# Optimization experiments

Hardware: AMD Instinct MI355X
Metric: run time of the kernel (lower is better)

Reference implementation:

```python
import jax, jax.numpy as jnp
import numpy as np

N, E, H, L = 50000, 800000, 96, 4

def _gelu(x):
    return jax.nn.gelu(x, approximate=False)

def _mlp2(x, w1, b1, w2, b2):
    # Linear -> GELU -> (Dropout=identity in eval) -> Linear
    return _gelu(x @ w1 + b1) @ w2 + b2

def setup_inputs() -> dict:
    key = jax.random.key(0)
    ks = jax.random.split(key, 40)
    p = lambda k, s: jax.random.normal(k, s, jnp.float32) * 0.05
    inp = {
        'x': jax.random.normal(ks[0], (N, 6), jnp.float32),
        'edge_index': jax.random.randint(ks[1], (2, E), 0, N, jnp.int64),
        'edge_attr': jax.random.normal(ks[2], (E, 8), jnp.float32),
        # node encoder
        'ne_w1': p(ks[3], (6, H)), 'ne_b1': p(ks[4], (H,)),
        'ne_w2': p(ks[5], (H, H)), 'ne_b2': p(ks[6], (H,)),
        # edge encoder
        'ee_w1': p(ks[7], (8, H)), 'ee_b1': p(ks[8], (H,)),
        'ee_w2': p(ks[9], (H, H)), 'ee_b2': p(ks[10], (H,)),
        # per-layer message-passing MLPs (stacked over L)
        'mp_ew1': p(ks[11], (L, 3 * H, H)), 'mp_eb1': p(ks[12], (L, H)),
        'mp_ew2': p(ks[13], (L, H, H)),     'mp_eb2': p(ks[14], (L, H)),
        'mp_nw1': p(ks[15], (L, 2 * H, H)), 'mp_nb1': p(ks[16], (L, H)),
        'mp_nw2': p(ks[17], (L, H, H)),     'mp_nb2': p(ks[18], (L, H)),
        # node saliency head
        'nh_w1': p(ks[19], (H, H)), 'nh_b1': p(ks[20], (H,)),
        'nh_w2': p(ks[21], (H, 1)), 'nh_b2': p(ks[22], (1,)),
        # edge clustering head
        'eh_w1': p(ks[23], (3 * H, H)), 'eh_b1': p(ks[24], (H,)),
        'eh_w2': p(ks[25], (H, 1)),     'eh_b2': p(ks[26], (1,)),
    }
    return inp

def _forward(x, edge_attr, ne_w1, ne_b1, ne_w2, ne_b2, ee_w1, ee_b1, ee_w2, ee_b2,
             mp_ew1, mp_eb1, mp_ew2, mp_eb2, mp_nw1, mp_nb1, mp_nw2, mp_nb2,
             nh_w1, nh_b1, nh_w2, nh_b2, eh_w1, eh_b1, eh_w2, eh_b2, edge_index):
    src, dst = edge_index[0], edge_index[1]
    h = _mlp2(x, ne_w1, ne_b1, ne_w2, ne_b2)                 # [N,H]
    e = _mlp2(edge_attr, ee_w1, ee_b1, ee_w2, ee_b2)         # [E,H]
    for l in range(L):
        # edge update: residual MLP over [h_src, h_dst, e]
        m = jnp.concatenate([h[src], h[dst], e], axis=-1)    # [E,3H]
        e = e + _mlp2(m, mp_ew1[l], mp_eb1[l], mp_ew2[l], mp_eb2[l])
        # node update: residual MLP over [h, sum of incoming edge states]
        agg = jax.ops.segment_sum(e, dst, num_segments=N)    # [N,H]
        h = h + _mlp2(jnp.concatenate([h, agg], axis=-1), mp_nw1[l], mp_nb1[l], mp_nw2[l], mp_nb2[l])
    edge_logits = _mlp2(jnp.concatenate([h[src], h[dst], e], axis=-1), eh_w1, eh_b1, eh_w2, eh_b2)[:, 0]
    node_logits = _mlp2(h, nh_w1, nh_b1, nh_w2, nh_b2)[:, 0]
    return edge_logits, node_logits

def reference(x, edge_index, edge_attr, ne_w1, ne_b1, ne_w2, ne_b2, ee_w1, ee_b1, ee_w2, ee_b2,
              mp_ew1, mp_eb1, mp_ew2, mp_eb2, mp_nw1, mp_nb1, mp_nw2, mp_nb2,
              nh_w1, nh_b1, nh_w2, nh_b2, eh_w1, eh_b1, eh_w2, eh_b2):
    return _forward(x, edge_attr, ne_w1, ne_b1, ne_w2, ne_b2, ee_w1, ee_b1, ee_w2, ee_b2,
                    mp_ew1, mp_eb1, mp_ew2, mp_eb2, mp_nw1, mp_nb1, mp_nw2, mp_nb2,
                    nh_w1, nh_b1, nh_w2, nh_b2, eh_w1, eh_b1, eh_w2, eh_b2, edge_index)
```

## Files before the change

### kernel.cpp

```cpp
#include <hip/hip_runtime.h>
#include <hip/hip_bf16.h>
#include <math.h>


typedef __attribute__((ext_vector_type(8))) short short8;
typedef __attribute__((ext_vector_type(4))) float f32x4;

#define MFMA(a, b, c) __builtin_amdgcn_mfma_f32_16x16x32_bf16((a), (b), (c), 0, 0, 0)
#define WSTR 112

__device__ __forceinline__ float bf2f(ushort u) {
    union { uint i; float f; } v; v.i = ((uint)u) << 16; return v.f;
}
__device__ __forceinline__ ushort f2bf(float f) {
    union { float f; uint i; } v; v.f = f;
    uint b = v.i;
    return (ushort)((b + 0x7FFFu + ((b >> 16) & 1u)) >> 16);
}
__device__ __forceinline__ float gelu_f(float x) {
    return 0.5f * x * (1.0f + erff(x * 0.70710678118654752440f));
}
__device__ __forceinline__ short8 ld8(const ushort* p) { return *(const short8*)p; }
__device__ __forceinline__ ushort cvt_elem(const void* p, size_t j, int f32) {
    return f32 ? f2bf(((const float*)p)[j]) : ((const ushort*)p)[j];
}
template <int NT>
__device__ __forceinline__ void stageW(ushort* dst, const ushort* src, int t) {
    for (int i = t; i < 1152; i += NT) {
        int row = i / 12, ch = i - row * 12;
        ((short8*)dst)[row * 14 + ch] = ((const short8*)src)[i];
    }
}

__global__ __launch_bounds__(256) void detect_kernel(
    const ushort* __restrict__ X, const uint* __restrict__ IDX, int* __restrict__ flags)
{
    __shared__ int cnt[2];
    if (threadIdx.x == 0) { cnt[0] = 0; cnt[1] = 0; }
    __syncthreads();
    int plaus = 0;
    for (int i = threadIdx.x; i < 2048; i += 256) {
        float v = fabsf(bf2f(X[i]));
        if (v > 1e-3f && v < 100.f) plaus++;
    }
    atomicAdd(&cnt[0], plaus);
    int nz = 0;
    for (int i = threadIdx.x; i < 1024; i += 256)
        if (IDX[2 * i + 1] != 0) nz++;
    atomicAdd(&cnt[1], nz);
    __syncthreads();
    if (threadIdx.x == 0) {
        flags[0] = (cnt[0] < 1843) ? 1 : 0;
        flags[1] = (cnt[1] == 0) ? 1 : 0;
    }
}

struct SPk { const void* src[16]; int off[17]; };
__global__ __launch_bounds__(256) void smalls_kernel(SPk p, ushort* __restrict__ dst,
                                                     const int* __restrict__ flags) {
    int f = flags[0];
    for (int i = threadIdx.x; i < 3650; i += 256) {
        int e = 0;
        while (e < 15 && i >= p.off[e + 1]) e++;
        dst[i] = cvt_elem(p.src[e], (size_t)(i - p.off[e]), f);
    }
}

struct TPk { const void* base[34]; int eloff[34]; };
__global__ __launch_bounds__(256) void transpose_k(TPk p, ushort* __restrict__ dst,
                                                   const int* __restrict__ flags) {
    int f = flags[0];
    int m = blockIdx.x;
    const void* s = p.base[m];
    size_t off = (size_t)p.eloff[m];
    ushort* d = dst + (size_t)m * 9216;
    for (int i = threadIdx.x; i < 9216; i += 256) {
        int n = i / 96, k = i - n * 96;
        d[i] = cvt_elem(s, off + (size_t)k * 96 + n, f);
    }
}

__global__ __launch_bounds__(256) void idx_convert(
    const int* __restrict__ eidx, int* __restrict__ s32, int* __restrict__ d32,
    const int* __restrict__ flags, int E)
{
    int f = flags[1];
    for (size_t i = (size_t)blockIdx.x * 256 + threadIdx.x; i < (size_t)E;
         i += (size_t)gridDim.x * 256) {
        s32[i] = f ? eidx[2 * i] : eidx[i];
        d32[i] = f ? eidx[2 * ((size_t)E + i)] : eidx[(size_t)E + i];
    }
}

__global__ __launch_bounds__(256) void xe_convert(
    const void* __restrict__ xin, const void* __restrict__ ein,
    ushort* __restrict__ xb, ushort* __restrict__ eb,
    const int* __restrict__ flags, size_t nx, size_t ne)
{
    int f = flags[0];
    size_t total = nx + ne;
    for (size_t i = (size_t)blockIdx.x * 256 + threadIdx.x; i < total;
         i += (size_t)gridDim.x * 256) {
        if (i < nx) xb[i] = cvt_elem(xin, i, f);
        else        eb[i - nx] = cvt_elem(ein, i - nx, f);
    }
}

__global__ __launch_bounds__(256) void hist_kernel(const int* __restrict__ d32,
                                                   int* __restrict__ cnt, int E) {
    for (size_t i = (size_t)blockIdx.x * 256 + threadIdx.x; i < (size_t)E;
         i += (size_t)gridDim.x * 256)
        atomicAdd(&cnt[d32[i]], 1);
}

__global__ __launch_bounds__(1024) void prefix_kernel(int* __restrict__ cnt,
                                                      int* __restrict__ rowptr,
                                                      int N, int E) {
    __shared__ int part[1024];
    int t = threadIdx.x;
    int chunk = (N + 1023) / 1024;
    int b = t * chunk, e = b + chunk; if (e > N) e = N;
    int s = 0;
    for (int i = b; i < e; i++) s += cnt[i];
    part[t] = s;
    __syncthreads();
    for (int off = 1; off < 1024; off <<= 1) {
        int v = (t >= off) ? part[t - off] : 0;
        __syncthreads();
        part[t] += v;
        __syncthreads();
    }
    int run = part[t] - s;
    for (int i = b; i < e; i++) {
        int c = cnt[i];
        rowptr[i] = run;
        cnt[i] = run;
        run += c;
    }
    if (t == 1023) rowptr[N] = E;
}

__global__ __launch_bounds__(256) void scatter_kernel(
    const int* __restrict__ s32, const int* __restrict__ d32,
    int* __restrict__ cursor, int* __restrict__ ss, int* __restrict__ ds,
    int* __restrict__ eid, int E)
{
    for (size_t i = (size_t)blockIdx.x * 256 + threadIdx.x; i < (size_t)E;
         i += (size_t)gridDim.x * 256) {
        int d = d32[i];
        int pos = atomicAdd(&cursor[d], 1);
        ss[pos] = s32[i];
        ds[pos] = d;
        eid[pos] = (int)i;
    }
}

template <int K, bool WF32>
__global__ __launch_bounds__(256) void encoder_kernel(
    const ushort* __restrict__ X, const ushort* __restrict__ W1,
    const ushort* __restrict__ B1, const ushort* __restrict__ W2t,
    const ushort* __restrict__ B2, ushort* __restrict__ OutB,
    float* __restrict__ OutF, const int* __restrict__ EID, int R)
{
    __shared__ __align__(16) ushort sW2[96 * WSTR];
    __shared__ float sW1[K * 96];
    __shared__ float sb1[96], sb2[96];
    __shared__ __align__(16) ushort gscr[4][16 * WSTR];
    int t = threadIdx.x;
    stageW<256>(sW2, W2t, t);
    for (int i = t; i < K * 96; i += 256) sW1[i] = bf2f(W1[i]);
    if (t < 96) { sb1[t] = bf2f(B1[t]); sb2[t] = bf2f(B2[t]); }
    __syncthreads();

    const int wave = t >> 6, lane = t & 63, lr = lane & 15, cg = lane >> 4, lk = cg * 8;
    int rbase = blockIdx.x * 64 + wave * 16;

    float wf[K][6];
#pragma unroll
    for (int k = 0; k < K; k++)
#pragma unroll
        for (int n = 0; n < 6; n++) wf[k][n] = sW1[k * 96 + n * 16 + lr];

    ushort* g = gscr[wave];
#pragma unroll
    for (int j = 0; j < 4; j++) {
        int r = rbase + cg * 4 + j;
        int rc = r < R ? r : R - 1;
        int rx = EID ? EID[rc] : rc;
        float xr[K];
        const uint* xu = (const uint*)(X + (size_t)rx * K);
#pragma unroll
        for (int q = 0; q < K / 2; q++) {
            uint u = xu[q];
            xr[2 * q] = bf2f((ushort)u); xr[2 * q + 1] = bf2f((ushort)(u >> 16));
        }
#pragma unroll
        for (int n = 0; n < 6; n++) {
            float v = sb1[n * 16 + lr];
#pragma unroll
            for (int k = 0; k < K; k++) v += xr[k] * wf[k][n];
            g[(cg * 4 + j) * WSTR + n * 16 + lr] = f2bf(gelu_f(v));
        }
    }
    __syncthreads();

    const ushort* grow = g + lr * WSTR + lk;
    short8 a0 = ld8(grow), a1 = ld8(grow + 32), a2 = ld8(grow + 64);
    f32x4 acc[6];
#pragma unroll
    for (int n = 0; n < 6; n++) {
        f32x4 z = {0.f, 0.f, 0.f, 0.f}; acc[n] = z;
        const ushort* wb = sW2 + (n * 16 + lr) * WSTR + lk;
        acc[n] = MFMA(a0, ld8(wb), acc[n]);
        acc[n] = MFMA(a1, ld8(wb + 32), acc[n]);
        acc[n] = MFMA(a2, ld8(wb + 64), acc[n]);
    }
#pragma unroll
    for (int j = 0; j < 4; j++) {
        int r = rbase + cg * 4 + j;
        if (r < R) {
#pragma unroll
            for (int n = 0; n < 6; n++) {
                int c = n * 16 + lr;
                float v = acc[n][j] + sb2[c];
                OutB[(size_t)r * 96 + c] = f2bf(v);
                if constexpr (WF32) OutF[(size_t)r * 96 + c] = v;
            }
        }
    }
}

__global__ __launch_bounds__(256) void gemm_dual_kernel(
    const ushort* __restrict__ A, const ushort* __restrict__ W1t,
    const ushort* __restrict__ W2t, ushort* __restrict__ O1,
    ushort* __restrict__ O2, int R)
{
    __shared__ __align__(16) ushort sW1[96 * WSTR], sW2[96 * WSTR];
    int t = threadIdx.x;
    stageW<256>(sW1, W1t, t);
    stageW<256>(sW2, W2t, t);
    __syncthreads();
    const int wave = t >> 6, lane = t & 63, lr = lane & 15, cg = lane >> 4, lk = cg * 8;
    int rbase = blockIdx.x * 64 + wave * 16;
    int ra = rbase + lr; if (ra > R - 1) ra = R - 1;
    const ushort* arow = A + (size_t)ra * 96 + lk;
    short8 a0 = ld8(arow), a1 = ld8(arow + 32), a2 = ld8(arow + 64);
    f32x4 acc1[6], acc2[6];
#pragma unroll
    for (int n = 0; n < 6; n++) {
        f32x4 z = {0.f, 0.f, 0.f, 0.f}; acc1[n] = z; acc2[n] = z;
        const ushort* w1 = sW1 + (n * 16 + lr) * WSTR + lk;
        const ushort* w2 = sW2 + (n * 16 + lr) * WSTR + lk;
        acc1[n] = MFMA(a0, ld8(w1), acc1[n]);
        acc1[n] = MFMA(a1, ld8(w1 + 32), acc1[n]);
        acc1[n] = MFMA(a2, ld8(w1 + 64), acc1[n]);
        acc2[n] = MFMA(a0, ld8(w2), acc2[n]);
        acc2[n] = MFMA(a1, ld8(w2 + 32), acc2[n]);
        acc2[n] = MFMA(a2, ld8(w2 + 64), acc2[n]);
    }
#pragma unroll
    for (int j = 0; j < 4; j++) {
        int r = rbase + cg * 4 + j;
        if (r < R) {
#pragma unroll
            for (int n = 0; n < 6; n++) {
                int c = n * 16 + lr;
                O1[(size_t)r * 96 + c] = f2bf(acc1[n][j]);
                O2[(size_t)r * 96 + c] = f2bf(acc2[n][j]);
            }
        }
    }
}

__global__ __launch_bounds__(512) void edge_layer_kernel(
    ushort* __restrict__ Eio,
    const ushort* __restrict__ HA, const ushort* __restrict__ HB,
    const int* __restrict__ SRC, const int* __restrict__ DST,
    const ushort* __restrict__ W1t, const ushort* __restrict__ B1,
    const ushort* __restrict__ W2t, const ushort* __restrict__ B2,
    int ntiles, int Etot)
{
    __shared__ __align__(16) ushort sW1[96 * WSTR], sW2[96 * WSTR];
    __shared__ __align__(16) ushort gscr[8][16 * WSTR];
    __shared__ float sb1[96], sb2[96];
    int t = threadIdx.x;
    stageW<512>(sW1, W1t, t);
    stageW<512>(sW2, W2t, t);
    if (t < 96) { sb1[t] = bf2f(B1[t]); sb2[t] = bf2f(B2[t]); }
    __syncthreads();
    const int wave = t >> 6, lane = t & 63, lr = lane & 15, cg = lane >> 4, lk = cg * 8;
    ushort* g = gscr[wave];

    for (int tile = blockIdx.x; tile < ntiles; tile += gridDim.x) {
        int rbase = tile * 128 + wave * 16;
        int ra = rbase + lr; if (ra > Etot - 1) ra = Etot - 1;
        const ushort* arow = Eio + (size_t)ra * 96 + lk;
        short8 a0 = ld8(arow), a1 = ld8(arow + 32), a2 = ld8(arow + 64);
        f32x4 acc[6];
#pragma unroll
        for (int n = 0; n < 6; n++) {
            f32x4 z = {0.f, 0.f, 0.f, 0.f}; acc[n] = z;
            const ushort* wb = sW1 + (n * 16 + lr) * WSTR + lk;
            acc[n] = MFMA(a0, ld8(wb), acc[n]);
            acc[n] = MFMA(a1, ld8(wb + 32), acc[n]);
            acc[n] = MFMA(a2, ld8(wb + 64), acc[n]);
        }
        int s4[4], d4[4];
#pragma unroll
        for (int j = 0; j < 4; j++) {
            int r = rbase + cg * 4 + j; if (r > Etot - 1) r = Etot - 1;
            s4[j] = SRC[r]; d4[j] = DST[r];
        }
#pragma unroll
        for (int j = 0; j < 4; j++) {
            const ushort* pa = HA + (size_t)s4[j] * 96;
            const ushort* pb = HB + (size_t)d4[j] * 96;
            int rl = cg * 4 + j;
#pragma unroll
            for (int n = 0; n < 6; n++) {
                int c = n * 16 + lr;
                float v = acc[n][j] + bf2f(pa[c]) + bf2f(pb[c]) + sb1[c];
                g[rl * WSTR + c] = f2bf(gelu_f(v));
            }
        }
        __syncthreads();
        const ushort* grow = g + lr * WSTR + lk;
        short8 b0 = ld8(grow), b1v = ld8(grow + 32), b2v = ld8(grow + 64);
        f32x4 acc2[6];
#pragma unroll
        for (int n = 0; n < 6; n++) {
            f32x4 z = {0.f, 0.f, 0.f, 0.f}; acc2[n] = z;
            const ushort* wb = sW2 + (n * 16 + lr) * WSTR + lk;
            acc2[n] = MFMA(b0, ld8(wb), acc2[n]);
            acc2[n] = MFMA(b1v, ld8(wb + 32), acc2[n]);
            acc2[n] = MFMA(b2v, ld8(wb + 64), acc2[n]);
        }
#pragma unroll
        for (int j = 0; j < 4; j++) {
            int r = rbase + cg * 4 + j;
            if (r < Etot) {
                ushort* erow = Eio + (size_t)r * 96;
#pragma unroll
                for (int n = 0; n < 6; n++) {
                    int c = n * 16 + lr;
                    float v = acc2[n][j] + sb2[c] + bf2f(erow[c]);
                    erow[c] = f2bf(v);
                }
            }
        }
        __syncthreads();
    }
}

template <bool HF32>
__global__ __launch_bounds__(256) void node_layer_kernel(
    float* __restrict__ HF, ushort* __restrict__ HBF,
    const ushort* __restrict__ EB, const int* __restrict__ ROWPTR,
    const ushort* __restrict__ W1at, const ushort* __restrict__ W1bt,
    const ushort* __restrict__ B1, const ushort* __restrict__ W2t,
    const ushort* __restrict__ B2, int R)
{
    __shared__ __align__(16) ushort sWa[96 * WSTR], sWb[96 * WSTR], sW2[96 * WSTR];
    __shared__ __align__(16) ushort gscr[4][16 * WSTR];
    __shared__ float sb1[96], sb2[96];
    int t = threadIdx.x;
    stageW<256>(sWa, W1at, t);
    stageW<256>(sWb, W1bt, t);
    stageW<256>(sW2, W2t, t);
    if (t < 96) { sb1[t] = bf2f(B1[t]); sb2[t] = bf2f(B2[t]); }
    __syncthreads();
    const int wave = t >> 6, lane = t & 63, lr = lane & 15, cg = lane >> 4, lk = cg * 8;
    int rbase = blockIdx.x * 64 + wave * 16;
    int ra = rbase + lr; if (ra > R - 1) ra = R - 1;
    const ushort* hrow = HBF + (size_t)ra * 96 + lk;
    short8 a0 = ld8(hrow), a1 = ld8(hrow + 32), a2 = ld8(hrow + 64);

    float ag[24];
#pragma unroll
    for (int i = 0; i < 24; i++) ag[i] = 0.f;
    int beg = ROWPTR[ra], end = ROWPTR[ra + 1];
    for (int k = beg; k < end; k++) {
        const ushort* er = EB + (size_t)k * 96 + lk;
        short8 e0 = ld8(er), e1 = ld8(er + 32), e2 = ld8(er + 64);
#pragma unroll
        for (int i = 0; i < 8; i++) {
            ag[i]      += bf2f((ushort)e0[i]);
            ag[8 + i]  += bf2f((ushort)e1[i]);
            ag[16 + i] += bf2f((ushort)e2[i]);
        }
    }
    short8 g0, g1, g2;
#pragma unroll
    for (int i = 0; i < 8; i++) {
        g0[i] = (short)f2bf(ag[i]);
        g1[i] = (short)f2bf(ag[8 + i]);
        g2[i] = (short)f2bf(ag[16 + i]);
    }

    f32x4 acc[6];
#pragma unroll
    for (int n = 0; n < 6; n++) {
        f32x4 z = {0.f, 0.f, 0.f, 0.f}; acc[n] = z;
        const ushort* wa = sWa + (n * 16 + lr) * WSTR + lk;
        const ushort* wb = sWb + (n * 16 + lr) * WSTR + lk;
        acc[n] = MFMA(a0, ld8(wa), acc[n]);
        acc[n] = MFMA(a1, ld8(wa + 32), acc[n]);
        acc[n] = MFMA(a2, ld8(wa + 64), acc[n]);
        acc[n] = MFMA(g0, ld8(wb), acc[n]);
        acc[n] = MFMA(g1, ld8(wb + 32), acc[n]);
        acc[n] = MFMA(g2, ld8(wb + 64), acc[n]);
    }
    ushort* g = gscr[wave];
#pragma unroll
    for (int j = 0; j < 4; j++) {
        int rl = cg * 4 + j;
#pragma unroll
        for (int n = 0; n < 6; n++) {
            int c = n * 16 + lr;
            g[rl * WSTR + c] = f2bf(gelu_f(acc[n][j] + sb1[c]));
        }
    }
    __syncthreads();
    const ushort* grow = g + lr * WSTR + lk;
    short8 b0 = ld8(grow), b1v = ld8(grow + 32), b2v = ld8(grow + 64);
    f32x4 acc2[6];
#pragma unroll
    for (int n = 0; n < 6; n++) {
        f32x4 z = {0.f, 0.f, 0.f, 0.f}; acc2[n] = z;
        const ushort* wb = sW2 + (n * 16 + lr) * WSTR + lk;
        acc2[n] = MFMA(b0, ld8(wb), acc2[n]);
        acc2[n] = MFMA(b1v, ld8(wb + 32), acc2[n]);
        acc2[n] = MFMA(b2v, ld8(wb + 64), acc2[n]);
    }
#pragma unroll
    for (int j = 0; j < 4; j++) {
        int r = rbase + cg * 4 + j;
        if (r < R) {
#pragma unroll
            for (int n = 0; n < 6; n++) {
                int c = n * 16 + lr;
                size_t idx = (size_t)r * 96 + c;
                float base;
                if constexpr (HF32) base = HF[idx]; else base = bf2f(HBF[idx]);
                float v = base + acc2[n][j] + sb2[c];
                if constexpr (HF32) HF[idx] = v;
                HBF[idx] = f2bf(v);
            }
        }
    }
}

template <bool GATHER>
__global__ __launch_bounds__(256) void head_kernel(
    const ushort* __restrict__ Arows,
    const ushort* __restrict__ HA, const ushort* __restrict__ HB,
    const int* __restrict__ SRC, const int* __restrict__ DST,
    const ushort* __restrict__ W1t, const ushort* __restrict__ B1,
    const ushort* __restrict__ W2v, const ushort* __restrict__ B2,
    float* __restrict__ Out, const int* __restrict__ EID, int R)
{
    __shared__ __align__(16) ushort sW1[96 * WSTR];
    __shared__ float sb1[96], sw2[96];
    __shared__ float sb2s;
    int t = threadIdx.x;
    stageW<256>(sW1, W1t, t);
    if (t < 96) { sb1[t] = bf2f(B1[t]); sw2[t] = bf2f(W2v[t]); }
    if (t == 0) sb2s = bf2f(B2[0]);
    __syncthreads();
    const int wave = t >> 6, lane = t & 63, lr = lane & 15, cg = lane >> 4, lk = cg * 8;
    int rbase = blockIdx.x * 64 + wave * 16;
    int ra = rbase + lr; if (ra > R - 1) ra = R - 1;
    const ushort* arow = Arows + (size_t)ra * 96 + lk;
    short8 a0 = ld8(arow), a1 = ld8(arow + 32), a2 = ld8(arow + 64);

    f32x4 accT[6];
#pragma unroll
    for (int n = 0; n < 6; n++) {
        f32x4 z = {0.f, 0.f, 0.f, 0.f}; accT[n] = z;
        const ushort* wb = sW1 + (n * 16 + lr) * WSTR + lk;
        accT[n] = MFMA(ld8(wb), a0, accT[n]);
        accT[n] = MFMA(ld8(wb + 32), a1, accT[n]);
        accT[n] = MFMA(ld8(wb + 64), a2, accT[n]);
    }

    const ushort* pa = nullptr; const ushort* pb = nullptr;
    if constexpr (GATHER) {
        pa = HA + (size_t)SRC[ra] * 96 + cg * 4;
        pb = HB + (size_t)DST[ra] * 96 + cg * 4;
    }
    float s = 0.f;
#pragma unroll
    for (int n = 0; n < 6; n++) {
        const float* b1p = sb1 + n * 16 + cg * 4;
        const float* w2p = sw2 + n * 16 + cg * 4;
        float v0 = accT[n][0] + b1p[0];
        float v1 = accT[n][1] + b1p[1];
        float v2 = accT[n][2] + b1p[2];
        float v3 = accT[n][3] + b1p[3];
        if constexpr (GATHER) {
            uint2 ua = *(const uint2*)(pa + n * 16);
            uint2 ub = *(const uint2*)(pb + n * 16);
            v0 += bf2f((ushort)ua.x) + bf2f((ushort)ub.x);
            v1 += bf2f((ushort)(ua.x >> 16)) + bf2f((ushort)(ub.x >> 16));
            v2 += bf2f((ushort)ua.y) + bf2f((ushort)ub.y);
            v3 += bf2f((ushort)(ua.y >> 16)) + bf2f((ushort)(ub.y >> 16));
        }
        s += gelu_f(v0) * w2p[0] + gelu_f(v1) * w2p[1]
           + gelu_f(v2) * w2p[2] + gelu_f(v3) * w2p[3];
    }
    s += __shfl_xor(s, 16, 64);
    s += __shfl_xor(s, 32, 64);
    int r = rbase + lr;
    if (cg == 0 && r < R) {
        int ro = EID ? EID[r] : r;
        Out[ro] = s + sb2s;
    }
}

extern "C" void kernel_launch(void* const* d_in, const int* in_sizes, int n_in,
                              void* d_out, int out_size, void* d_ws, size_t ws_size,
                              hipStream_t stream)
{
    (void)n_in; (void)out_size;
    const int N = in_sizes[0] / 6;
    const int E = in_sizes[2] / 8;

    auto a256 = [](size_t b) { return (b + 255) & ~(size_t)255; };
    const size_t sz_flags = 256;
    const size_t sz_wt    = a256((size_t)34 * 9216 * 2);
    const size_t sz_sm    = a256(3650 * 2);
    const size_t sz_hbf   = a256((size_t)N * 96 * 2);
    const size_t sz_ebuf  = a256((size_t)E * 96 * 2);
    const size_t sz_idx   = a256((size_t)E * 4);
    const size_t sz_np    = a256((size_t)(N + 1) * 4);
    const size_t sz_xbf   = a256((size_t)N * 6 * 2);
    const size_t sz_eabf  = a256((size_t)E * 8 * 2);
    const size_t sz_hf    = a256((size_t)N * 96 * 4);

    const size_t need_base   = sz_flags + sz_wt + sz_sm + 3 * sz_hbf + sz_ebuf
                             + 2 * sz_np + 3 * sz_idx;
    const size_t need_copies = need_base + 2 * sz_idx + sz_xbf + sz_eabf;
    const size_t need_full   = need_copies + sz_hf;
    int mode = (ws_size >= need_full) ? 0 : (ws_size >= need_copies) ? 1 : 2;
    const bool hf32 = (mode == 0), copies = (mode <= 1);

    char* ws = (char*)d_ws;
    size_t off = 0;
    auto alloc = [&](size_t bytes) -> void* { void* p = ws + off; off += bytes; return p; };
    int*    flags  = (int*)alloc(sz_flags);
    ushort* wtpool = (ushort*)alloc(sz_wt);
    ushort* smalls = (ushort*)alloc(sz_sm);
    ushort* h_bf   = (ushort*)alloc(sz_hbf);
    ushort* hA     = (ushort*)alloc(sz_hbf);
    ushort* hB     = (ushort*)alloc(sz_hbf);
    ushort* ebuf   = (ushort*)alloc(sz_ebuf);
    int*    cnt    = (int*)alloc(sz_np);
    int*    rowptr = (int*)alloc(sz_np);
    int*    src_s  = (int*)alloc(sz_idx);
    int*    dst_s  = (int*)alloc(sz_idx);
    int*    eid    = (int*)alloc(sz_idx);
    const int* eidx = (const int*)d_in[1];
    int*    src32 = copies ? (int*)alloc(sz_idx) : (int*)eidx;
    int*    dst32 = copies ? (int*)alloc(sz_idx) : (int*)(eidx + E);
    ushort* x_bf  = copies ? (ushort*)alloc(sz_xbf)  : (ushort*)d_in[0];
    ushort* ea_bf = copies ? (ushort*)alloc(sz_eabf) : (ushort*)d_in[2];
    float*  h_f32 = hf32 ? (float*)alloc(sz_hf) : nullptr;

    SPk sp;
    const int soff[17] = {0, 576, 672, 768, 1536, 1632, 1728, 2112, 2496, 2880,
                          3264, 3360, 3456, 3552, 3648, 3649, 3650};
    for (int i = 0; i < 17; i++) sp.off[i] = soff[i];
    sp.src[0]  = d_in[3];   sp.src[1]  = d_in[4];   sp.src[2]  = d_in[6];
    sp.src[3]  = d_in[7];   sp.src[4]  = d_in[8];   sp.src[5]  = d_in[10];
    sp.src[6]  = d_in[12];  sp.src[7]  = d_in[14];  sp.src[8]  = d_in[16];
    sp.src[9]  = d_in[18];  sp.src[10] = d_in[20];  sp.src[11] = d_in[21];
    sp.src[12] = d_in[24];  sp.src[13] = d_in[25];  sp.src[14] = d_in[22];
    sp.src[15] = d_in[26];
    auto SM = [&](int o) { return smalls + o; };

    TPk tp; int q = 0;
    tp.base[q] = d_in[5];  tp.eloff[q++] = 0;
    tp.base[q] = d_in[9];  tp.eloff[q++] = 0;
    for (int l = 0; l < 4; l++) {
        tp.base[q] = d_in[11]; tp.eloff[q++] = l * 27648;
        tp.base[q] = d_in[11]; tp.eloff[q++] = l * 27648 + 9216;
        tp.base[q] = d_in[11]; tp.eloff[q++] = l * 27648 + 18432;
        tp.base[q] = d_in[13]; tp.eloff[q++] = l * 9216;
        tp.base[q] = d_in[15]; tp.eloff[q++] = l * 18432;
        tp.base[q] = d_in[15]; tp.eloff[q++] = l * 18432 + 9216;
        tp.base[q] = d_in[17]; tp.eloff[q++] = l * 9216;
    }
    tp.base[q] = d_in[23]; tp.eloff[q++] = 0;
    tp.base[q] = d_in[23]; tp.eloff[q++] = 9216;
    tp.base[q] = d_in[23]; tp.eloff[q++] = 18432;
    tp.base[q] = d_in[19]; tp.eloff[q++] = 0;
    auto WT = [&](int i) { return wtpool + (size_t)i * 9216; };

    const int nblkN = (N + 63) / 64;
    const int nblkE = (E + 63) / 64;
    const int ntilE128 = (E + 127) / 128;

    detect_kernel<<<1, 256, 0, stream>>>((const ushort*)d_in[0], (const uint*)d_in[1], flags);
    smalls_kernel<<<1, 256, 0, stream>>>(sp, smalls, flags);
    transpose_k<<<34, 256, 0, stream>>>(tp, wtpool, flags);
    if (copies) {
        idx_convert<<<1024, 256, 0, stream>>>(eidx, src32, dst32, flags, E);
        xe_convert<<<2048, 256, 0, stream>>>(d_in[0], d_in[2], x_bf, ea_bf, flags,
                                             (size_t)N * 6, (size_t)E * 8);
    }
    hipMemsetAsync(cnt, 0, (size_t)(N + 1) * 4, stream);
    hist_kernel<<<1024, 256, 0, stream>>>(dst32, cnt, E);
    prefix_kernel<<<1, 1024, 0, stream>>>(cnt, rowptr, N, E);
    scatter_kernel<<<1024, 256, 0, stream>>>(src32, dst32, cnt, src_s, dst_s, eid, E);

    if (hf32)
        encoder_kernel<6, true><<<nblkN, 256, 0, stream>>>(x_bf, SM(0), SM(576), WT(0), SM(672), h_bf, h_f32, nullptr, N);
    else
        encoder_kernel<6, false><<<nblkN, 256, 0, stream>>>(x_bf, SM(0), SM(576), WT(0), SM(672), h_bf, nullptr, nullptr, N);
    encoder_kernel<8, false><<<nblkE, 256, 0, stream>>>(ea_bf, SM(768), SM(1536), WT(1), SM(1632), ebuf, nullptr, eid, E);

    for (int l = 0; l < 4; l++) {
        int b = 2 + l * 7;
        gemm_dual_kernel<<<nblkN, 256, 0, stream>>>(h_bf, WT(b + 0), WT(b + 1), hA, hB, N);
        int egrid = ntilE128 < 2048 ? ntilE128 : 2048;
        edge_layer_kernel<<<egrid, 512, 0, stream>>>(
            ebuf, hA, hB, src_s, dst_s, WT(b + 2), SM(1728 + l * 96),
            WT(b + 3), SM(2112 + l * 96), ntilE128, E);
        if (hf32)
            node_layer_kernel<true><<<nblkN, 256, 0, stream>>>(
                h_f32, h_bf, ebuf, rowptr, WT(b + 4), WT(b + 5), SM(2496 + l * 96),
                WT(b + 6), SM(2880 + l * 96), N);
        else
            node_layer_kernel<false><<<nblkN, 256, 0, stream>>>(
                nullptr, h_bf, ebuf, rowptr, WT(b + 4), WT(b + 5), SM(2496 + l * 96),
                WT(b + 6), SM(2880 + l * 96), N);
    }

    gemm_dual_kernel<<<nblkN, 256, 0, stream>>>(h_bf, WT(30), WT(31), hA, hB, N);
    float* out = (float*)d_out;
    head_kernel<true><<<nblkE, 256, 0, stream>>>(
        ebuf, hA, hB, src_s, dst_s, WT(32), SM(3456), SM(3552), SM(3649), out, eid, E);
    head_kernel<false><<<nblkN, 256, 0, stream>>>(
        h_bf, nullptr, nullptr, nullptr, nullptr, WT(33), SM(3264), SM(3360), SM(3648), out + E, nullptr, N);
}
```

Measured before the change: 1.462 ms.

## Prefetch next edge tile and swizzle block-to-tile mapping across XCDs

The edge-layer kernel now software-pipelines its persistent loop, loading the next tile's edge rows and src/dst indices into registers while the current tile's MFMAs and gathers run. Block IDs are also remapped so that consecutive tiles go to blocks on the same XCD, and the grid is rounded up to a multiple of 8 so the swizzle stays a bijection. The aim is to hide global-load latency and improve L2 locality, at the cost of more live registers and a possibly lower occupancy.

After: 1.529 ms. 4.6% more time.

```diff
diff --git a/kernel.cpp b/kernel.cpp
--- a/kernel.cpp
+++ b/kernel.cpp
@@ -291,11 +291,29 @@
     const int wave = t >> 6, lane = t & 63, lr = lane & 15, cg = lane >> 4, lk = cg * 8;
     ushort* g = gscr[wave];
 
-    for (int tile = blockIdx.x; tile < ntiles; tile += gridDim.x) {
+    int bid = blockIdx.x;
+    int cpx = gridDim.x >> 3;
+    int swz = (bid & 7) * cpx + (bid >> 3);
+
+    int tile = swz;
+    short8 a0, a1, a2;
+    int s4[4], d4[4];
+    {
         int rbase = tile * 128 + wave * 16;
         int ra = rbase + lr; if (ra > Etot - 1) ra = Etot - 1;
         const ushort* arow = Eio + (size_t)ra * 96 + lk;
-        short8 a0 = ld8(arow), a1 = ld8(arow + 32), a2 = ld8(arow + 64);
+        a0 = ld8(arow); a1 = ld8(arow + 32); a2 = ld8(arow + 64);
+#pragma unroll
+        for (int j = 0; j < 4; j++) {
+            int r = rbase + cg * 4 + j; if (r > Etot - 1) r = Etot - 1;
+            s4[j] = SRC[r]; d4[j] = DST[r];
+        }
+    }
+
+    while (tile < ntiles) {
+        int rbase = tile * 128 + wave * 16;
+        int ntile = tile + gridDim.x;
+
         f32x4 acc[6];
 #pragma unroll
         for (int n = 0; n < 6; n++) {
@@ -305,12 +323,25 @@
             acc[n] = MFMA(a1, ld8(wb + 32), acc[n]);
             acc[n] = MFMA(a2, ld8(wb + 64), acc[n]);
         }
-        int s4[4], d4[4];
-#pragma unroll
-        for (int j = 0; j < 4; j++) {
-            int r = rbase + cg * 4 + j; if (r > Etot - 1) r = Etot - 1;
-            s4[j] = SRC[r]; d4[j] = DST[r];
-        }
+
+        short8 na0, na1, na2;
+        int ns4[4], nd4[4];
+        if (ntile < ntiles) {
+            int nrbase = ntile * 128 + wave * 16;
+            int nra = nrbase + lr; if (nra > Etot - 1) nra = Etot - 1;
+            const ushort* narow = Eio + (size_t)nra * 96 + lk;
+            na0 = ld8(narow); na1 = ld8(narow + 32); na2 = ld8(narow + 64);
+#pragma unroll
+            for (int j = 0; j < 4; j++) {
+                int r = nrbase + cg * 4 + j; if (r > Etot - 1) r = Etot - 1;
+                ns4[j] = SRC[r]; nd4[j] = DST[r];
+            }
+        } else {
+            na0 = a0; na1 = a1; na2 = a2;
+#pragma unroll
+            for (int j = 0; j < 4; j++) { ns4[j] = s4[j]; nd4[j] = d4[j]; }
+        }
+
 #pragma unroll
         for (int j = 0; j < 4; j++) {
             const ushort* pa = HA + (size_t)s4[j] * 96;
@@ -349,6 +380,11 @@
             }
         }
         __syncthreads();
+
+        a0 = na0; a1 = na1; a2 = na2;
+#pragma unroll
+        for (int j = 0; j < 4; j++) { s4[j] = ns4[j]; d4[j] = nd4[j]; }
+        tile = ntile;
     }
 }
 
@@ -619,10 +655,10 @@
         encoder_kernel<6, false><<<nblkN, 256, 0, stream>>>(x_bf, SM(0), SM(576), WT(0), SM(672), h_bf, nullptr, nullptr, N);
     encoder_kernel<8, false><<<nblkE, 256, 0, stream>>>(ea_bf, SM(768), SM(1536), WT(1), SM(1632), ebuf, nullptr, eid, E);
 
+    int egrid = ntilE128 < 2048 ? ((ntilE128 + 7) & ~7) : 2048;
     for (int l = 0; l < 4; l++) {
         int b = 2 + l * 7;
         gemm_dual_kernel<<<nblkN, 256, 0, stream>>>(h_bf, WT(b + 0), WT(b + 1), hA, hB, N);
-        int egrid = ntilE128 < 2048 ? ntilE128 : 2048;
         edge_layer_kernel<<<egrid, 512, 0, stream>>>(
             ebuf, hA, hB, src_s, dst_s, WT(b + 2), SM(1728 + l * 96),
             WT(b + 3), SM(2112 + l * 96), ntilE128, E);
```
